# Performance work log

Measured on AMD Instinct MI355X. Metric: run time of the kernel, lower is better.

## Reference

```python
import jax, jax.numpy as jnp
import numpy as np

K = 6            # kmer length
NF = 8192        # n_filters (> 4**K so kmer_params has shape (NF, 4, K))
M = 4 ** K       # 4096 kmers
B = 1024         # batch


def setup_inputs() -> dict:
    key = jax.random.key(0)
    k1, k2 = jax.random.split(key)
    freq = jax.random.uniform(k1, (B, M), dtype=jnp.float32)          # kmer frequencies (B, 4^k)
    kmer_params = jax.random.normal(k2, (NF, 4, K), dtype=jnp.float32)
    temperature = jnp.ones((1,), dtype=jnp.float32)
    # base-4 digits of arange(4^k), most-significant first == itertools.product order
    pos = 4 ** jnp.arange(K - 1, -1, -1)
    kmer_idcs = ((jnp.arange(M)[:, None] // pos[None, :]) % 4).astype(jnp.int32)  # (M, K)
    return {"freq": freq, "kmer_params": kmer_params,
            "temperature": temperature, "kmer_idcs": kmer_idcs}


def reference(freq, kmer_params, temperature, kmer_idcs):
    k = kmer_params.shape[-1]
    # matches[f, i] = sum_j kmer_params[f, kmer_idcs[i, j], j]
    # Advanced indexing broadcasts (M, k) indices against arange(k): result (F, M, k).
    # This replaces torch's expand-to-(F, M, 1, k) + gather + squeeze + sum(-1).
    matches = kmer_params[:, kmer_idcs, jnp.arange(k)].sum(axis=-1)   # (F, M)
    probs = jax.nn.softmax(matches / temperature, axis=1)             # softmax over kmers
    pooled = freq @ probs.T                                           # (B, F)
    profile = pooled / pooled.sum(axis=1, keepdims=True)
    return profile
```

## Files before the change

### kernel.cpp

```cpp
#include <hip/hip_runtime.h>


typedef __bf16  bf16x8 __attribute__((ext_vector_type(8)));
typedef float   f32x4  __attribute__((ext_vector_type(4)));

#define GLD16(gp, lp)                                                          \
  __builtin_amdgcn_global_load_lds(                                            \
      (const __attribute__((address_space(1))) void*)(gp),                     \
      (__attribute__((address_space(3))) void*)(lp), 16, 0, 0)

__device__ __forceinline__ short f2bf(float x) {
  unsigned u = __float_as_uint(x);
  unsigned r = (u + 0x7fffu + ((u >> 16) & 1u)) >> 16;
  return (short)r;
}

__device__ __forceinline__ float wave_max(float v) {
  #pragma unroll
  for (int off = 32; off; off >>= 1) v = fmaxf(v, __shfl_xor(v, off, 64));
  return v;
}
__device__ __forceinline__ float wave_sum(float v) {
  #pragma unroll
  for (int off = 32; off; off >>= 1) v += __shfl_xor(v, off, 64);
  return v;
}

__global__ __launch_bounds__(256) void cast_kernel(const float* __restrict__ in,
                                                   short* __restrict__ out) {
  int idx = blockIdx.x * 256 + threadIdx.x;
  float4 v = ((const float4*)in)[idx];
  short4 o;
  o.x = f2bf(v.x); o.y = f2bf(v.y); o.z = f2bf(v.z); o.w = f2bf(v.w);
  ((short4*)out)[idx] = o;
}

__global__ __launch_bounds__(256) void tables_kernel(const float* __restrict__ kp,
                                                     const float* __restrict__ temp,
                                                     float* __restrict__ E1t,
                                                     float* __restrict__ E2) {
  const int t = threadIdx.x;
  const int lane = t & 63, wave = t >> 6;
  const int f = blockIdx.x * 4 + wave;
  const float* P = kp + f * 24;
  const int d0 = (lane >> 4) & 3, d1 = (lane >> 2) & 3, d2 = lane & 3;
  const float thi = P[d0 * 6 + 0] + P[d1 * 6 + 1] + P[d2 * 6 + 2];
  const float tlo = P[d0 * 6 + 3] + P[d1 * 6 + 4] + P[d2 * 6 + 5];
  const float mxhi = wave_max(thi), mxlo = wave_max(tlo);
  const float invT = 1.0f / temp[0];
  const float e1 = __expf((thi - mxhi) * invT);
  const float e2 = __expf((tlo - mxlo) * invT);
  const float s1 = wave_sum(e1), s2 = wave_sum(e2);
  const float invZ = 1.0f / (s1 * s2);
  E1t[lane * 8192 + f] = e1 * invZ;
  E2[(size_t)f * 64 + lane] = e2;
}

__global__ __launch_bounds__(256, 4) void gemm_kernel(const short* __restrict__ A,
                                                      const float* __restrict__ E1t,
                                                      const float* __restrict__ E2,
                                                      float* __restrict__ C) {
  __shared__ short As[64 * 64];

  const int t = threadIdx.x;
  const int lane = t & 63, wave = t >> 6;
  const int quad = lane >> 4, l16 = lane & 15;
  const int m0 = blockIdx.y * 64;
  const int n0 = blockIdx.x * 128;
  const int wn = wave * 32;

  f32x4 acc[4][2];
  #pragma unroll
  for (int i = 0; i < 4; i++)
    #pragma unroll
    for (int j = 0; j < 2; j++) acc[i][j] = (f32x4){0.f, 0.f, 0.f, 0.f};

  int nrow[2];
  #pragma unroll
  for (int j = 0; j < 2; j++) nrow[j] = n0 + wn + j * 16 + l16;
  float4 e2a[2][2], e2b[2][2];
  #pragma unroll
  for (int j = 0; j < 2; j++)
    #pragma unroll
    for (int ks = 0; ks < 2; ks++) {
      const float* p = E2 + (size_t)nrow[j] * 64 + (ks * 4 + quad) * 8;
      e2a[j][ks] = *(const float4*)p;
      e2b[j][ks] = *(const float4*)(p + 4);
    }

  const int lane_row = lane >> 3;
  const int src_col = ((lane & 7) ^ lane_row) * 8;
  const int sw = l16 & 7;

  for (int kt = 0; kt < 64; kt++) {
    const int kofs = kt * 64;
    float e1v[2];
    #pragma unroll
    for (int j = 0; j < 2; j++) e1v[j] = E1t[kt * 8192 + nrow[j]];

    __syncthreads();
    #pragma unroll
    for (int c = 0; c < 2; c++) {
      const int chunk = wave * 2 + c;
      const int row = chunk * 8 + lane_row;
      GLD16(A + (m0 + row) * 4096 + kofs + src_col, &As[chunk * 512 + lane * 8]);
    }
    __syncthreads();

    bf16x8 b[2][2];
    #pragma unroll
    for (int j = 0; j < 2; j++)
      #pragma unroll
      for (int ks = 0; ks < 2; ks++) {
        const float s = e1v[j];
        bf16x8 bb;
        bb[0] = (__bf16)(s * e2a[j][ks].x);
        bb[1] = (__bf16)(s * e2a[j][ks].y);
        bb[2] = (__bf16)(s * e2a[j][ks].z);
        bb[3] = (__bf16)(s * e2a[j][ks].w);
        bb[4] = (__bf16)(s * e2b[j][ks].x);
        bb[5] = (__bf16)(s * e2b[j][ks].y);
        bb[6] = (__bf16)(s * e2b[j][ks].z);
        bb[7] = (__bf16)(s * e2b[j][ks].w);
        b[ks][j] = bb;
      }

    #pragma unroll
    for (int ks = 0; ks < 2; ks++) {
      const int pcol = ((ks * 4 + quad) ^ sw) * 8;
      bf16x8 a[4];
      #pragma unroll
      for (int i = 0; i < 4; i++)
        a[i] = *(const bf16x8*)&As[(i * 16 + l16) * 64 + pcol];
      #pragma unroll
      for (int i = 0; i < 4; i++)
        #pragma unroll
        for (int j = 0; j < 2; j++)
          acc[i][j] = __builtin_amdgcn_mfma_f32_16x16x32_bf16(a[i], b[ks][j], acc[i][j], 0, 0, 0);
    }
  }

  #pragma unroll
  for (int i = 0; i < 4; i++) {
    #pragma unroll
    for (int r = 0; r < 4; r++) {
      const int brow = m0 + i * 16 + quad * 4 + r;
      float* crow = C + (size_t)brow * 8192 + n0 + wn + l16;
      #pragma unroll
      for (int j = 0; j < 2; j++) crow[j * 16] = acc[i][j][r];
    }
  }
}

__global__ __launch_bounds__(256) void norm_kernel(float* __restrict__ out) {
  const int b = blockIdx.x;
  const int t = threadIdx.x;
  const int lane = t & 63, wave = t >> 6;
  __shared__ float red[4];

  float4* row = (float4*)(out + (size_t)b * 8192);
  float4 v[8];
  float s = 0.0f;
  #pragma unroll
  for (int q = 0; q < 8; q++) {
    v[q] = row[q * 256 + t];
    s += (v[q].x + v[q].y) + (v[q].z + v[q].w);
  }
  float ws = wave_sum(s);
  if (lane == 0) red[wave] = ws;
  __syncthreads();
  float tot = (red[0] + red[1]) + (red[2] + red[3]);
  float inv = 1.0f / tot;
  #pragma unroll
  for (int q = 0; q < 8; q++) {
    v[q].x *= inv; v[q].y *= inv; v[q].z *= inv; v[q].w *= inv;
    row[q * 256 + t] = v[q];
  }
}

extern "C" void kernel_launch(void* const* d_in, const int* in_sizes, int n_in,
                              void* d_out, int out_size, void* d_ws, size_t ws_size,
                              hipStream_t stream) {
  const float* freq    = (const float*)d_in[0];
  const float* kparams = (const float*)d_in[1];
  const float* temp    = (const float*)d_in[2];

  float* out = (float*)d_out;

  short* freqb = (short*)d_ws;
  float* E1t   = (float*)(freqb + (size_t)1024 * 4096);
  float* E2    = E1t + (size_t)64 * 8192;

  cast_kernel  <<<4096, 256, 0, stream>>>(freq, freqb);
  tables_kernel<<<2048, 256, 0, stream>>>(kparams, temp, E1t, E2);
  gemm_kernel  <<<dim3(64, 16), 256, 0, stream>>>(freqb, E1t, E2, out);
  norm_kernel  <<<1024, 256, 0, stream>>>(out);
}
```

Baseline: 164.6 us.

## Enlarge GEMM tiles and triple-buffer A loads with software pipelining

The GEMM block tile grows from 64x128 with 4 waves to 128x256 with 8 waves, each wave now computing a 64x64 subtile. The freq tile is loaded into a 3-stage LDS ring two iterations ahead, with vmcnt-based waits and one barrier per iteration. The next E1 scale is prefetched into registers, and s_setprio raises wave priority around the MFMA bursts. The aim is more reuse of the on-the-fly B fragments and of A per LDS load, and hiding global latency. The cost is higher register pressure and only 256 blocks, which may leave CUs underused.

```diff
diff --git a/kernel.cpp b/kernel.cpp
--- a/kernel.cpp
+++ b/kernel.cpp
@@ -56,31 +56,32 @@
   E2[(size_t)f * 64 + lane] = e2;
 }
 
-__global__ __launch_bounds__(256, 4) void gemm_kernel(const short* __restrict__ A,
+__global__ __launch_bounds__(512, 2) void gemm_kernel(const short* __restrict__ A,
                                                       const float* __restrict__ E1t,
                                                       const float* __restrict__ E2,
                                                       float* __restrict__ C) {
-  __shared__ short As[64 * 64];
+  __shared__ short As[3 * 128 * 64];
 
   const int t = threadIdx.x;
   const int lane = t & 63, wave = t >> 6;
   const int quad = lane >> 4, l16 = lane & 15;
-  const int m0 = blockIdx.y * 64;
-  const int n0 = blockIdx.x * 128;
-  const int wn = wave * 32;
-
-  f32x4 acc[4][2];
+  const int m0 = blockIdx.y * 128;
+  const int n0 = blockIdx.x * 256;
+  const int wm = (wave >> 2) * 64;
+  const int wn = (wave & 3) * 64;
+
+  f32x4 acc[4][4];
   #pragma unroll
   for (int i = 0; i < 4; i++)
     #pragma unroll
-    for (int j = 0; j < 2; j++) acc[i][j] = (f32x4){0.f, 0.f, 0.f, 0.f};
-
-  int nrow[2];
-  #pragma unroll
-  for (int j = 0; j < 2; j++) nrow[j] = n0 + wn + j * 16 + l16;
-  float4 e2a[2][2], e2b[2][2];
-  #pragma unroll
-  for (int j = 0; j < 2; j++)
+    for (int j = 0; j < 4; j++) acc[i][j] = (f32x4){0.f, 0.f, 0.f, 0.f};
+
+  int nrow[4];
+  #pragma unroll
+  for (int j = 0; j < 4; j++) nrow[j] = n0 + wn + j * 16 + l16;
+  float4 e2a[4][2], e2b[4][2];
+  #pragma unroll
+  for (int j = 0; j < 4; j++)
     #pragma unroll
     for (int ks = 0; ks < 2; ks++) {
       const float* p = E2 + (size_t)nrow[j] * 64 + (ks * 4 + quad) * 8;
@@ -92,27 +93,53 @@
   const int src_col = ((lane & 7) ^ lane_row) * 8;
   const int sw = l16 & 7;
 
-  for (int kt = 0; kt < 64; kt++) {
-    const int kofs = kt * 64;
-    float e1v[2];
-    #pragma unroll
-    for (int j = 0; j < 2; j++) e1v[j] = E1t[kt * 8192 + nrow[j]];
-
-    __syncthreads();
-    #pragma unroll
-    for (int c = 0; c < 2; c++) {
-      const int chunk = wave * 2 + c;
-      const int row = chunk * 8 + lane_row;
-      GLD16(A + (m0 + row) * 4096 + kofs + src_col, &As[chunk * 512 + lane * 8]);
-    }
-    __syncthreads();
-
-    bf16x8 b[2][2];
-    #pragma unroll
-    for (int j = 0; j < 2; j++)
+  const int r0 = wave * 16;
+  const short* Abase = A + (size_t)(m0 + r0 + lane_row) * 4096 + src_col;
+
+  #define STAGE(kt, buf) do {                                                  \
+    const short* g_ = Abase + (kt) * 64;                                       \
+    GLD16(g_,            &As[(buf) * 8192 + r0 * 64 + lane * 8]);              \
+    GLD16(g_ + 8 * 4096, &As[(buf) * 8192 + (r0 + 8) * 64 + lane * 8]);        \
+  } while (0)
+
+  float e1n[4], e1c[4];
+  STAGE(0, 0);
+  #pragma unroll
+  for (int j = 0; j < 4; j++) e1n[j] = E1t[nrow[j]];
+  STAGE(1, 1);
+
+  int cb = 0, sb = 2;
+
+  #pragma unroll 1
+  for (int kt = 0; kt < 64; ++kt) {
+    asm volatile("s_waitcnt vmcnt(2)" ::: "memory");
+    __builtin_amdgcn_s_barrier();
+    asm volatile("" ::: "memory");
+
+    #pragma unroll
+    for (int j = 0; j < 4; j++) e1c[j] = e1n[j];
+    const int tn = (kt + 1 > 63) ? 63 : kt + 1;
+    #pragma unroll
+    for (int j = 0; j < 4; j++) e1n[j] = E1t[tn * 8192 + nrow[j]];
+    const int ts = (kt + 2 > 63) ? 63 : kt + 2;
+    STAGE(ts, sb);
+
+    const short* buf = &As[cb * 8192];
+
+    bf16x8 a[4][2];
+    #pragma unroll
+    for (int i = 0; i < 4; i++)
+      #pragma unroll
+      for (int ks = 0; ks < 2; ks++)
+        a[i][ks] = *(const bf16x8*)&buf[(wm + i * 16 + l16) * 64 +
+                                        (((ks * 4 + quad) ^ sw) * 8)];
+
+    #pragma unroll
+    for (int j = 0; j < 4; j++) {
+      bf16x8 b[2];
       #pragma unroll
       for (int ks = 0; ks < 2; ks++) {
-        const float s = e1v[j];
+        const float s = e1c[j];
         bf16x8 bb;
         bb[0] = (__bf16)(s * e2a[j][ks].x);
         bb[1] = (__bf16)(s * e2a[j][ks].y);
@@ -122,34 +149,35 @@
         bb[5] = (__bf16)(s * e2b[j][ks].y);
         bb[6] = (__bf16)(s * e2b[j][ks].z);
         bb[7] = (__bf16)(s * e2b[j][ks].w);
-        b[ks][j] = bb;
+        b[ks] = bb;
       }
-
-    #pragma unroll
-    for (int ks = 0; ks < 2; ks++) {
-      const int pcol = ((ks * 4 + quad) ^ sw) * 8;
-      bf16x8 a[4];
-      #pragma unroll
-      for (int i = 0; i < 4; i++)
-        a[i] = *(const bf16x8*)&As[(i * 16 + l16) * 64 + pcol];
-      #pragma unroll
-      for (int i = 0; i < 4; i++)
+      __builtin_amdgcn_s_setprio(1);
+      #pragma unroll
+      for (int ks = 0; ks < 2; ks++)
         #pragma unroll
-        for (int j = 0; j < 2; j++)
-          acc[i][j] = __builtin_amdgcn_mfma_f32_16x16x32_bf16(a[i], b[ks][j], acc[i][j], 0, 0, 0);
+        for (int i = 0; i < 4; i++)
+          acc[i][j] = __builtin_amdgcn_mfma_f32_16x16x32_bf16(a[i][ks], b[ks],
+                                                              acc[i][j], 0, 0, 0);
+      __builtin_amdgcn_s_setprio(0);
     }
-  }
+
+    cb = (cb + 1 == 3) ? 0 : cb + 1;
+    sb = (sb + 1 == 3) ? 0 : sb + 1;
+  }
+
+  asm volatile("s_waitcnt vmcnt(0)" ::: "memory");
 
   #pragma unroll
   for (int i = 0; i < 4; i++) {
     #pragma unroll
     for (int r = 0; r < 4; r++) {
-      const int brow = m0 + i * 16 + quad * 4 + r;
+      const int brow = m0 + wm + i * 16 + quad * 4 + r;
       float* crow = C + (size_t)brow * 8192 + n0 + wn + l16;
       #pragma unroll
-      for (int j = 0; j < 2; j++) crow[j * 16] = acc[i][j][r];
+      for (int j = 0; j < 4; j++) crow[j * 16] = acc[i][j][r];
     }
   }
+  #undef STAGE
 }
 
 __global__ __launch_bounds__(256) void norm_kernel(float* __restrict__ out) {
@@ -193,6 +221,6 @@
 
   cast_kernel  <<<4096, 256, 0, stream>>>(freq, freqb);
   tables_kernel<<<2048, 256, 0, stream>>>(kparams, temp, E1t, E2);
-  gemm_kernel  <<<dim3(64, 16), 256, 0, stream>>>(freqb, E1t, E2, out);
+  gemm_kernel  <<<dim3(32, 8), 512, 0, stream>>>(freqb, E1t, E2, out);
   norm_kernel  <<<1024, 256, 0, stream>>>(out);
 }
```

Result: slower. 179.6 us (+9.1%).
